# Performance work log

Hardware: AMD Instinct MI355X
Metric: run time of the kernel (lower is better)

Reference implementation:

```python
import jax, jax.numpy as jnp
import numpy as np

N_STATE = 1024
N_HEAD = 16
DIM_PER_HEAD = N_STATE // N_HEAD  # 64
QK_SCALE = DIM_PER_HEAD ** (-0.5)
B, T, T_CACHE = 8, 256, 768


def setup_inputs() -> dict:
    key = jax.random.key(0)
    ks = jax.random.split(key, 12)
    s = 0.02
    return {
        "x": jax.random.normal(ks[0], (B, T, N_STATE), dtype=jnp.float32),
        "qk_mask": jnp.zeros((T, T_CACHE + T), dtype=jnp.float32),
        "cache_k": jax.random.normal(ks[1], (B, T_CACHE, N_STATE), dtype=jnp.float32),
        "cache_v": jax.random.normal(ks[2], (B, T_CACHE, N_STATE), dtype=jnp.float32),
        "Wq": jax.random.normal(ks[3], (N_STATE, N_STATE), dtype=jnp.float32) * s,
        "bq": jax.random.normal(ks[4], (N_STATE,), dtype=jnp.float32) * s,
        "Wk": jax.random.normal(ks[5], (N_STATE, N_STATE), dtype=jnp.float32) * s,
        "Wv": jax.random.normal(ks[6], (N_STATE, N_STATE), dtype=jnp.float32) * s,
        "bv": jax.random.normal(ks[7], (N_STATE,), dtype=jnp.float32) * s,
        "Wo": jax.random.normal(ks[8], (N_STATE, N_STATE), dtype=jnp.float32) * s,
        "bo": jax.random.normal(ks[9], (N_STATE,), dtype=jnp.float32) * s,
    }


def reference(x, qk_mask, cache_k, cache_v, Wq, bq, Wk, Wv, bv, Wo, bo):
    # Linear projections (weights stored as [in, out], i.e. torch weight^T)
    q = (x @ Wq + bq) * QK_SCALE            # [B, T, D]
    new_k = x @ Wk                           # key has no bias
    new_v = x @ Wv + bv
    # KV-cache concat along time
    k = jnp.concatenate([cache_k, new_k], axis=1)  # [B, Tkv, D]
    v = jnp.concatenate([cache_v, new_v], axis=1)
    # Split heads
    Bq, Tq = q.shape[:2]
    Tkv = k.shape[1]
    qh = q.reshape(Bq, Tq, N_HEAD, DIM_PER_HEAD)    # [B, T, H, d]
    kh = k.reshape(Bq, Tkv, N_HEAD, DIM_PER_HEAD)
    vh = v.reshape(Bq, Tkv, N_HEAD, DIM_PER_HEAD)
    # q @ k^T + mask, softmax over keys
    qk = jnp.einsum("bthd,bshd->bhts", qh, kh) + qk_mask  # [B, H, T, Tkv]
    w = jax.nn.softmax(qk, axis=-1).astype(qh.dtype)
    wv = jnp.einsum("bhts,bshd->bthd", w, vh).reshape(Bq, Tq, N_STATE)
    out = wv @ Wo + bo
    return out, new_k, new_v
```

## Files before the change

kernel.cpp:

```cpp
#include <hip/hip_runtime.h>
#include <hip/hip_bf16.h>
#include <stdint.h>

#define Bb 8
#define Tt 256
#define TCC 768
#define TKV 1024
#define NS 1024
#define NH 16
#define DH 64
#define QK_SCALE 0.125f

typedef short bf16x8 __attribute__((ext_vector_type(8)));
typedef float f32x4 __attribute__((ext_vector_type(4)));

__device__ __forceinline__ unsigned short f2bf(float f) {
  union { float f; uint32_t u; } v; v.f = f;
  uint32_t u = v.u;
  u += 0x7fff + ((u >> 16) & 1);
  return (unsigned short)(u >> 16);
}

__global__ void convert_flat(const float* __restrict__ x, const float* __restrict__ ck,
                             unsigned short* __restrict__ xb, unsigned short* __restrict__ kb) {
  const int64_t nx4 = (int64_t)Bb * Tt * NS / 4;
  const int64_t nk4 = (int64_t)Bb * TCC * NS / 4;
  int64_t stride = (int64_t)gridDim.x * blockDim.x;
  for (int64_t t = (int64_t)blockIdx.x * blockDim.x + threadIdx.x; t < nx4 + nk4; t += stride) {
    if (t < nx4) {
      float4 v = ((const float4*)x)[t];
      ushort4 o; o.x = f2bf(v.x); o.y = f2bf(v.y); o.z = f2bf(v.z); o.w = f2bf(v.w);
      ((ushort4*)xb)[t] = o;
    } else {
      int64_t e = t - nx4;
      float4 v = ((const float4*)ck)[e];
      ushort4 o; o.x = f2bf(v.x); o.y = f2bf(v.y); o.z = f2bf(v.z); o.w = f2bf(v.w);
      int64_t el = e * 4;
      int64_t b = el / ((int64_t)TCC * NS);
      int64_t rem = el % ((int64_t)TCC * NS);
      int64_t d = b * (int64_t)TKV * NS + rem;
      ((ushort4*)kb)[d / 4] = o;
    }
  }
}

__global__ void transpose_convert(const float* __restrict__ Wq, const float* __restrict__ Wk,
                                  const float* __restrict__ Wv, const float* __restrict__ Wo,
                                  const float* __restrict__ cv,
                                  unsigned short* __restrict__ wqt, unsigned short* __restrict__ wkt,
                                  unsigned short* __restrict__ wvt, unsigned short* __restrict__ wot,
                                  unsigned short* __restrict__ vbt) {
  __shared__ float tile[64][65];
  int bid = blockIdx.x;
  const float* src; unsigned short* dst;
  if (bid < 1024) {
    int mat = bid >> 8, t = bid & 255;
    int tr = t >> 4, tc = t & 15;
    const float* W = (mat == 0) ? Wq : (mat == 1) ? Wk : (mat == 2) ? Wv : Wo;
    unsigned short* Wt = (mat == 0) ? wqt : (mat == 1) ? wkt : (mat == 2) ? wvt : wot;
    src = W + (int64_t)(tr * 64) * 1024 + tc * 64;
    dst = Wt + (int64_t)(tc * 64) * 1024 + tr * 64;
  } else {
    int e = bid - 1024;
    int b = e / 192; int t = e % 192;
    int st = t >> 4, ct = t & 15;
    src = cv + (int64_t)b * TCC * NS + (int64_t)(st * 64) * 1024 + ct * 64;
    dst = vbt + (int64_t)b * NS * TKV + (int64_t)(ct * 64) * 1024 + st * 64;
  }
  for (int e = threadIdx.x; e < 4096; e += 256) {
    int i = e >> 6, j = e & 63;
    tile[i][j] = src[(int64_t)i * 1024 + j];
  }
  __syncthreads();
  for (int e = threadIdx.x; e < 4096; e += 256) {
    int i = e >> 6, j = e & 63;
    dst[(int64_t)i * 1024 + j] = f2bf(tile[j][i]);
  }
}

template <int MODE>
__global__ void gemm128(const unsigned short* __restrict__ A,
                        const unsigned short* __restrict__ Bt0, const unsigned short* __restrict__ Bt1,
                        const unsigned short* __restrict__ Bt2,
                        const float* __restrict__ bq, const float* __restrict__ bv,
                        const float* __restrict__ bo,
                        unsigned short* __restrict__ qb,
                        float* __restrict__ okf, float* __restrict__ ovf,
                        unsigned short* __restrict__ kb, unsigned short* __restrict__ vbt,
                        float* __restrict__ outf) {
  __shared__ unsigned short As[128 * 40];
  __shared__ unsigned short Bs[128 * 40];
  int tid = threadIdx.x, lane = tid & 63, w = tid >> 6;
  int lr = lane & 15, hi = lane >> 4;
  int wr = w >> 1, wc = w & 1;

  int tm, seg, col0;
  const unsigned short* Bt;
  if (MODE == 0) {
    tm = blockIdx.x & 15; int tn = blockIdx.x >> 4;
    seg = tn >> 3; col0 = (tn & 7) * 128;
    Bt = (seg == 0) ? Bt0 : (seg == 1) ? Bt1 : Bt2;
  } else {
    tm = blockIdx.x & 15; int tn = blockIdx.x >> 4;
    seg = 0; col0 = tn * 128;
    Bt = Bt0;
  }
  int m0 = tm * 128;

  f32x4 acc[4][4];
#pragma unroll
  for (int i = 0; i < 4; i++)
#pragma unroll
    for (int j = 0; j < 4; j++) acc[i][j] = (f32x4){0.f, 0.f, 0.f, 0.f};

  for (int k0 = 0; k0 < 1024; k0 += 32) {
#pragma unroll
    for (int e = tid; e < 512; e += 256) {
      int r = e >> 2, kc = (e & 3) * 8;
      *(bf16x8*)&As[r * 40 + kc] = *(const bf16x8*)&A[(int64_t)(m0 + r) * 1024 + k0 + kc];
      *(bf16x8*)&Bs[r * 40 + kc] = *(const bf16x8*)&Bt[(int64_t)(col0 + r) * 1024 + k0 + kc];
    }
    __syncthreads();
    bf16x8 af[4], bf[4];
#pragma unroll
    for (int mt = 0; mt < 4; mt++) af[mt] = *(const bf16x8*)&As[(wr * 64 + mt * 16 + lr) * 40 + hi * 8];
#pragma unroll
    for (int nt = 0; nt < 4; nt++) bf[nt] = *(const bf16x8*)&Bs[(wc * 64 + nt * 16 + lr) * 40 + hi * 8];
#pragma unroll
    for (int mt = 0; mt < 4; mt++)
#pragma unroll
      for (int nt = 0; nt < 4; nt++)
        acc[mt][nt] = __builtin_amdgcn_mfma_f32_16x16x32_bf16(af[mt], bf[nt], acc[mt][nt], 0, 0, 0);
    __syncthreads();
  }

#pragma unroll
  for (int mt = 0; mt < 4; mt++)
#pragma unroll
    for (int nt = 0; nt < 4; nt++) {
      int row = m0 + wr * 64 + mt * 16 + hi * 4;
      int col = col0 + wc * 64 + nt * 16 + lr;
      if (MODE == 1) {
        float bias = bo[col];
#pragma unroll
        for (int r = 0; r < 4; r++)
          outf[(int64_t)(row + r) * 1024 + col] = acc[mt][nt][r] + bias;
      } else if (seg == 0) {
        float bias = bq[col];
#pragma unroll
        for (int r = 0; r < 4; r++)
          qb[(int64_t)(row + r) * 1024 + col] = f2bf((acc[mt][nt][r] + bias) * QK_SCALE);
      } else if (seg == 1) {
#pragma unroll
        for (int r = 0; r < 4; r++) {
          float v = acc[mt][nt][r];
          okf[(int64_t)(row + r) * 1024 + col] = v;
          int b = (row + r) >> 8, t = (row + r) & 255;
          kb[((int64_t)(b * TKV + TCC + t)) * 1024 + col] = f2bf(v);
        }
      } else {
        float bias = bv[col];
        int b = row >> 8, t0 = row & 255;
        int64_t voff = ((int64_t)(b * NH + (col >> 6)) * DH + (col & 63)) * TKV + TCC + t0;
        ushort4 pk;
        float v0 = acc[mt][nt][0] + bias, v1 = acc[mt][nt][1] + bias,
              v2 = acc[mt][nt][2] + bias, v3 = acc[mt][nt][3] + bias;
        ovf[(int64_t)(row + 0) * 1024 + col] = v0;
        ovf[(int64_t)(row + 1) * 1024 + col] = v1;
        ovf[(int64_t)(row + 2) * 1024 + col] = v2;
        ovf[(int64_t)(row + 3) * 1024 + col] = v3;
        pk.x = f2bf(v0); pk.y = f2bf(v1); pk.z = f2bf(v2); pk.w = f2bf(v3);
        *(ushort4*)&vbt[voff] = pk;
      }
    }
}

__global__ void attn(const unsigned short* __restrict__ qb, const unsigned short* __restrict__ kb,
                     const unsigned short* __restrict__ vbt, const float* __restrict__ mask,
                     unsigned short* __restrict__ wvb) {
  __shared__ unsigned short Ks[64 * 72];
  __shared__ unsigned short Vs[64 * 72];
  __shared__ unsigned short Ps[4][16 * 72];
  int tid = threadIdx.x, lane = tid & 63, w = tid >> 6;
  int lr = lane & 15, hi = lane >> 4;
  int qblk = blockIdx.x & 3, bh = blockIdx.x >> 2, b = bh >> 4, h = bh & 15;
  int q0 = qblk * 64 + w * 16;

  const unsigned short* qp = qb + ((int64_t)(b * Tt + q0 + lr)) * 1024 + h * DH + hi * 8;
  bf16x8 aq0 = *(const bf16x8*)qp;
  bf16x8 aq1 = *(const bf16x8*)(qp + 32);

  f32x4 o[4];
#pragma unroll
  for (int nt = 0; nt < 4; nt++) o[nt] = (f32x4){0.f, 0.f, 0.f, 0.f};
  float m[4] = {-1e30f, -1e30f, -1e30f, -1e30f};
  float l[4] = {0.f, 0.f, 0.f, 0.f};

  const unsigned short* kbase = kb + (int64_t)b * TKV * 1024 + h * DH;
  const unsigned short* vbase = vbt + (int64_t)bh * DH * TKV;
  const float* mbase = mask + (int64_t)(q0 + hi * 4) * TKV;

  for (int c = 0; c < 16; c++) {
    int kv0 = c * 64;
#pragma unroll
    for (int e = tid; e < 512; e += 256) {
      int r = e >> 3, kc = (e & 7) * 8;
      *(bf16x8*)&Ks[r * 72 + kc] = *(const bf16x8*)&kbase[(int64_t)(kv0 + r) * 1024 + kc];
      *(bf16x8*)&Vs[r * 72 + kc] = *(const bf16x8*)&vbase[(int64_t)r * TKV + kv0 + kc];
    }
    __syncthreads();

    f32x4 s[4];
#pragma unroll
    for (int nt = 0; nt < 4; nt++) {
      bf16x8 bk0 = *(const bf16x8*)&Ks[(nt * 16 + lr) * 72 + hi * 8];
      bf16x8 bk1 = *(const bf16x8*)&Ks[(nt * 16 + lr) * 72 + 32 + hi * 8];
      f32x4 z = (f32x4){0.f, 0.f, 0.f, 0.f};
      z = __builtin_amdgcn_mfma_f32_16x16x32_bf16(aq0, bk0, z, 0, 0, 0);
      z = __builtin_amdgcn_mfma_f32_16x16x32_bf16(aq1, bk1, z, 0, 0, 0);
      s[nt] = z;
    }
#pragma unroll
    for (int nt = 0; nt < 4; nt++)
#pragma unroll
      for (int r = 0; r < 4; r++)
        s[nt][r] += mbase[(int64_t)r * TKV + kv0 + nt * 16 + lr];

    float cm[4];
#pragma unroll
    for (int r = 0; r < 4; r++) {
      cm[r] = fmaxf(fmaxf(s[0][r], s[1][r]), fmaxf(s[2][r], s[3][r]));
#pragma unroll
      for (int d = 1; d < 16; d <<= 1) cm[r] = fmaxf(cm[r], __shfl_xor(cm[r], d));
    }
    float al[4], rs[4];
#pragma unroll
    for (int r = 0; r < 4; r++) {
      float nm = fmaxf(m[r], cm[r]);
      al[r] = __expf(m[r] - nm);
      m[r] = nm;
      rs[r] = 0.f;
    }
#pragma unroll
    for (int nt = 0; nt < 4; nt++)
#pragma unroll
      for (int r = 0; r < 4; r++) {
        s[nt][r] = __expf(s[nt][r] - m[r]);
        rs[r] += s[nt][r];
      }
#pragma unroll
    for (int r = 0; r < 4; r++) {
#pragma unroll
      for (int d = 1; d < 16; d <<= 1) rs[r] += __shfl_xor(rs[r], d);
      l[r] = l[r] * al[r] + rs[r];
    }
#pragma unroll
    for (int nt = 0; nt < 4; nt++)
#pragma unroll
      for (int r = 0; r < 4; r++) o[nt][r] *= al[r];

#pragma unroll
    for (int nt = 0; nt < 4; nt++)
#pragma unroll
      for (int r = 0; r < 4; r++)
        Ps[w][(hi * 4 + r) * 72 + nt * 16 + lr] = f2bf(s[nt][r]);
    __syncthreads();

    bf16x8 pa0 = *(const bf16x8*)&Ps[w][lr * 72 + hi * 8];
    bf16x8 pa1 = *(const bf16x8*)&Ps[w][lr * 72 + 32 + hi * 8];
#pragma unroll
    for (int nt = 0; nt < 4; nt++) {
      bf16x8 bv0 = *(const bf16x8*)&Vs[(nt * 16 + lr) * 72 + hi * 8];
      bf16x8 bv1 = *(const bf16x8*)&Vs[(nt * 16 + lr) * 72 + 32 + hi * 8];
      o[nt] = __builtin_amdgcn_mfma_f32_16x16x32_bf16(pa0, bv0, o[nt], 0, 0, 0);
      o[nt] = __builtin_amdgcn_mfma_f32_16x16x32_bf16(pa1, bv1, o[nt], 0, 0, 0);
    }
    __syncthreads();
  }

  float inv[4];
#pragma unroll
  for (int r = 0; r < 4; r++) inv[r] = 1.f / l[r];
#pragma unroll
  for (int nt = 0; nt < 4; nt++)
#pragma unroll
    for (int r = 0; r < 4; r++)
      wvb[(int64_t)(b * Tt + q0 + hi * 4 + r) * 1024 + h * DH + nt * 16 + lr] =
          f2bf(o[nt][r] * inv[r]);
}

extern "C" void kernel_launch(void* const* d_in, const int* in_sizes, int n_in,
                              void* d_out, int out_size, void* d_ws, size_t ws_size,
                              hipStream_t stream) {
  const float* x    = (const float*)d_in[0];
  const float* mask = (const float*)d_in[1];
  const float* ck   = (const float*)d_in[2];
  const float* cv   = (const float*)d_in[3];
  const float* Wq   = (const float*)d_in[4];
  const float* bq   = (const float*)d_in[5];
  const float* Wk   = (const float*)d_in[6];
  const float* Wv   = (const float*)d_in[7];
  const float* bv   = (const float*)d_in[8];
  const float* Wo   = (const float*)d_in[9];
  const float* bo   = (const float*)d_in[10];

  const int64_t NT = (int64_t)Bb * Tt * NS;
  float* outp = (float*)d_out;
  float* okf  = outp + NT;
  float* ovf  = outp + 2 * NT;

  char* ws = (char*)d_ws;
  unsigned short* xb  = (unsigned short*)(ws);
  unsigned short* wqt = (unsigned short*)(ws + (4LL << 20));
  unsigned short* wkt = (unsigned short*)(ws + (6LL << 20));
  unsigned short* wvt = (unsigned short*)(ws + (8LL << 20));
  unsigned short* wot = (unsigned short*)(ws + (10LL << 20));
  unsigned short* qbw = (unsigned short*)(ws + (12LL << 20));
  unsigned short* kbw = (unsigned short*)(ws + (16LL << 20));
  unsigned short* vbt = (unsigned short*)(ws + (32LL << 20));
  unsigned short* wvb = (unsigned short*)(ws + (48LL << 20));

  convert_flat<<<2048, 256, 0, stream>>>(x, ck, xb, kbw);
  transpose_convert<<<2560, 256, 0, stream>>>(Wq, Wk, Wv, Wo, cv, wqt, wkt, wvt, wot, vbt);
  gemm128<0><<<384, 256, 0, stream>>>(xb, wqt, wkt, wvt, bq, bv, bo,
                                      qbw, okf, ovf, kbw, vbt, outp);
  attn<<<512, 256, 0, stream>>>(qbw, kbw, vbt, mask, wvb);
  gemm128<1><<<128, 256, 0, stream>>>(wvb, wot, wot, wot, bq, bv, bo,
                                      qbw, okf, ovf, kbw, vbt, outp);
}
```

Baseline: 242.7 us.

## Double-buffer GEMM and attention tiles via direct global-to-LDS loads with swizzle

Both GEMMs are retiled to smaller blocks: 64x128 for the QKV projection and 64x64 for the output projection. They now stage K-chunks of 64 into double-buffered LDS using global_load_lds with an XOR-swizzled layout, so the next tile loads while MFMAs run on the current one. The attention kernel likewise double-buffers its K/V tiles, prefetches mask values, and drops the barrier around the per-wave P buffer. Block indices are remapped across the 8 XCDs and the weight/V transposes use vectorized float4/ushort4 accesses. This relies on the compiler inserting correct waits for the async LDS loads, and the smaller tiles reduce per-block data reuse in exchange for more blocks.

```diff
diff --git a/kernel.cpp b/kernel.cpp
--- a/kernel.cpp
+++ b/kernel.cpp
@@ -13,6 +13,7 @@
 
 typedef short bf16x8 __attribute__((ext_vector_type(8)));
 typedef float f32x4 __attribute__((ext_vector_type(4)));
+typedef unsigned int u32;
 
 __device__ __forceinline__ unsigned short f2bf(float f) {
   union { float f; uint32_t u; } v; v.f = f;
@@ -21,8 +22,16 @@
   return (unsigned short)(u >> 16);
 }
 
-__global__ void convert_flat(const float* __restrict__ x, const float* __restrict__ ck,
-                             unsigned short* __restrict__ xb, unsigned short* __restrict__ kb) {
+__device__ __forceinline__ void gload16(const unsigned short* g, unsigned short* l) {
+  __builtin_amdgcn_global_load_lds(
+      (__attribute__((address_space(1))) u32*)g,
+      (__attribute__((address_space(3))) u32*)l,
+      16, 0, 0);
+}
+
+__global__ __launch_bounds__(256) void convert_flat(
+    const float* __restrict__ x, const float* __restrict__ ck,
+    unsigned short* __restrict__ xb, unsigned short* __restrict__ kb) {
   const int64_t nx4 = (int64_t)Bb * Tt * NS / 4;
   const int64_t nk4 = (int64_t)Bb * TCC * NS / 4;
   int64_t stride = (int64_t)gridDim.x * blockDim.x;
@@ -44,12 +53,13 @@
   }
 }
 
-__global__ void transpose_convert(const float* __restrict__ Wq, const float* __restrict__ Wk,
-                                  const float* __restrict__ Wv, const float* __restrict__ Wo,
-                                  const float* __restrict__ cv,
-                                  unsigned short* __restrict__ wqt, unsigned short* __restrict__ wkt,
-                                  unsigned short* __restrict__ wvt, unsigned short* __restrict__ wot,
-                                  unsigned short* __restrict__ vbt) {
+__global__ __launch_bounds__(256) void transpose_convert(
+    const float* __restrict__ Wq, const float* __restrict__ Wk,
+    const float* __restrict__ Wv, const float* __restrict__ Wo,
+    const float* __restrict__ cv,
+    unsigned short* __restrict__ wqt, unsigned short* __restrict__ wkt,
+    unsigned short* __restrict__ wvt, unsigned short* __restrict__ wot,
+    unsigned short* __restrict__ vbt) {
   __shared__ float tile[64][65];
   int bid = blockIdx.x;
   const float* src; unsigned short* dst;
@@ -67,79 +77,117 @@
     src = cv + (int64_t)b * TCC * NS + (int64_t)(st * 64) * 1024 + ct * 64;
     dst = vbt + (int64_t)b * NS * TKV + (int64_t)(ct * 64) * 1024 + st * 64;
   }
-  for (int e = threadIdx.x; e < 4096; e += 256) {
-    int i = e >> 6, j = e & 63;
-    tile[i][j] = src[(int64_t)i * 1024 + j];
+  for (int e = threadIdx.x; e < 1024; e += 256) {
+    int i = e >> 4, j4 = (e & 15) * 4;
+    float4 v = *(const float4*)&src[(int64_t)i * 1024 + j4];
+    tile[i][j4] = v.x; tile[i][j4 + 1] = v.y; tile[i][j4 + 2] = v.z; tile[i][j4 + 3] = v.w;
   }
   __syncthreads();
-  for (int e = threadIdx.x; e < 4096; e += 256) {
-    int i = e >> 6, j = e & 63;
-    dst[(int64_t)i * 1024 + j] = f2bf(tile[j][i]);
+  for (int e = threadIdx.x; e < 1024; e += 256) {
+    int i = e >> 4, j4 = (e & 15) * 4;
+    ushort4 o;
+    o.x = f2bf(tile[j4][i]); o.y = f2bf(tile[j4 + 1][i]);
+    o.z = f2bf(tile[j4 + 2][i]); o.w = f2bf(tile[j4 + 3][i]);
+    *(ushort4*)&dst[(int64_t)i * 1024 + j4] = o;
   }
 }
 
 template <int MODE>
-__global__ void gemm128(const unsigned short* __restrict__ A,
-                        const unsigned short* __restrict__ Bt0, const unsigned short* __restrict__ Bt1,
-                        const unsigned short* __restrict__ Bt2,
-                        const float* __restrict__ bq, const float* __restrict__ bv,
-                        const float* __restrict__ bo,
-                        unsigned short* __restrict__ qb,
-                        float* __restrict__ okf, float* __restrict__ ovf,
-                        unsigned short* __restrict__ kb, unsigned short* __restrict__ vbt,
-                        float* __restrict__ outf) {
-  __shared__ unsigned short As[128 * 40];
-  __shared__ unsigned short Bs[128 * 40];
+__global__ __launch_bounds__(256) void gemm_mfma(
+    const unsigned short* __restrict__ A,
+    const unsigned short* __restrict__ Bt0, const unsigned short* __restrict__ Bt1,
+    const unsigned short* __restrict__ Bt2,
+    const float* __restrict__ bq, const float* __restrict__ bv,
+    const float* __restrict__ bo,
+    unsigned short* __restrict__ qb,
+    float* __restrict__ okf, float* __restrict__ ovf,
+    unsigned short* __restrict__ kb, unsigned short* __restrict__ vbt,
+    float* __restrict__ outf) {
+  constexpr int BM = 64;
+  constexpr int BN = (MODE == 0) ? 128 : 64;
+  constexpr int MT = 2;
+  constexpr int NTf = BN / 32;
+  __shared__ __align__(16) unsigned short As[2][BM * 64];
+  __shared__ __align__(16) unsigned short Bs[2][BN * 64];
+
   int tid = threadIdx.x, lane = tid & 63, w = tid >> 6;
   int lr = lane & 15, hi = lane >> 4;
-  int wr = w >> 1, wc = w & 1;
-
-  int tm, seg, col0;
+  int wm = w >> 1, wn = w & 1;
+
+  int bid = blockIdx.x;
+  int cpx = gridDim.x >> 3;
+  int logical = (bid & 7) * cpx + (bid >> 3);
+
+  int tm = logical & 31;
+  int tn = logical >> 5;
+  int seg, col0;
   const unsigned short* Bt;
   if (MODE == 0) {
-    tm = blockIdx.x & 15; int tn = blockIdx.x >> 4;
     seg = tn >> 3; col0 = (tn & 7) * 128;
     Bt = (seg == 0) ? Bt0 : (seg == 1) ? Bt1 : Bt2;
   } else {
-    tm = blockIdx.x & 15; int tn = blockIdx.x >> 4;
-    seg = 0; col0 = tn * 128;
+    seg = 0; col0 = tn * 64;
     Bt = Bt0;
   }
-  int m0 = tm * 128;
-
-  f32x4 acc[4][4];
-#pragma unroll
-  for (int i = 0; i < 4; i++)
-#pragma unroll
-    for (int j = 0; j < 4; j++) acc[i][j] = (f32x4){0.f, 0.f, 0.f, 0.f};
-
-  for (int k0 = 0; k0 < 1024; k0 += 32) {
-#pragma unroll
-    for (int e = tid; e < 512; e += 256) {
-      int r = e >> 2, kc = (e & 3) * 8;
-      *(bf16x8*)&As[r * 40 + kc] = *(const bf16x8*)&A[(int64_t)(m0 + r) * 1024 + k0 + kc];
-      *(bf16x8*)&Bs[r * 40 + kc] = *(const bf16x8*)&Bt[(int64_t)(col0 + r) * 1024 + k0 + kc];
-    }
+  int m0 = tm * 64;
+
+  int srow = lane >> 3;
+  int sch8 = (((lane & 7) ^ srow)) * 8;
+  int sw = lr & 7;
+
+  f32x4 acc[MT][NTf];
+#pragma unroll
+  for (int i = 0; i < MT; i++)
+#pragma unroll
+    for (int j = 0; j < NTf; j++) acc[i][j] = (f32x4){0.f, 0.f, 0.f, 0.f};
+
+  auto STAGE = [&](int buf, int k0) {
+#pragma unroll
+    for (int i = 0; i < 2; i++) {
+      int rb = w * 16 + i * 8;
+      gload16(&A[(int64_t)(m0 + rb + srow) * 1024 + k0 + sch8], &As[buf][rb * 64]);
+    }
+#pragma unroll
+    for (int i = 0; i < BN / 32; i++) {
+      int rb = w * (BN / 4) + i * 8;
+      gload16(&Bt[(int64_t)(col0 + rb + srow) * 1024 + k0 + sch8], &Bs[buf][rb * 64]);
+    }
+  };
+
+  STAGE(0, 0);
+  __syncthreads();
+  int cur = 0;
+  for (int step = 0; step < 16; ++step) {
+    if (step < 15) STAGE(cur ^ 1, (step + 1) * 64);
+    bf16x8 af[2][MT], bfr[2][NTf];
+#pragma unroll
+    for (int kk = 0; kk < 2; kk++) {
+      int ch = ((kk * 4 + hi) ^ sw) * 8;
+#pragma unroll
+      for (int mt = 0; mt < MT; mt++)
+        af[kk][mt] = *(const bf16x8*)&As[cur][(wm * 32 + mt * 16 + lr) * 64 + ch];
+#pragma unroll
+      for (int nt = 0; nt < NTf; nt++)
+        bfr[kk][nt] = *(const bf16x8*)&Bs[cur][(wn * (BN / 2) + nt * 16 + lr) * 64 + ch];
+    }
+#pragma unroll
+    for (int kk = 0; kk < 2; kk++)
+#pragma unroll
+      for (int mt = 0; mt < MT; mt++)
+#pragma unroll
+        for (int nt = 0; nt < NTf; nt++)
+          acc[mt][nt] = __builtin_amdgcn_mfma_f32_16x16x32_bf16(af[kk][mt], bfr[kk][nt],
+                                                               acc[mt][nt], 0, 0, 0);
     __syncthreads();
-    bf16x8 af[4], bf[4];
-#pragma unroll
-    for (int mt = 0; mt < 4; mt++) af[mt] = *(const bf16x8*)&As[(wr * 64 + mt * 16 + lr) * 40 + hi * 8];
-#pragma unroll
-    for (int nt = 0; nt < 4; nt++) bf[nt] = *(const bf16x8*)&Bs[(wc * 64 + nt * 16 + lr) * 40 + hi * 8];
-#pragma unroll
-    for (int mt = 0; mt < 4; mt++)
-#pragma unroll
-      for (int nt = 0; nt < 4; nt++)
-        acc[mt][nt] = __builtin_amdgcn_mfma_f32_16x16x32_bf16(af[mt], bf[nt], acc[mt][nt], 0, 0, 0);
-    __syncthreads();
-  }
-
-#pragma unroll
-  for (int mt = 0; mt < 4; mt++)
-#pragma unroll
-    for (int nt = 0; nt < 4; nt++) {
-      int row = m0 + wr * 64 + mt * 16 + hi * 4;
-      int col = col0 + wc * 64 + nt * 16 + lr;
+    cur ^= 1;
+  }
+
+#pragma unroll
+  for (int mt = 0; mt < MT; mt++)
+#pragma unroll
+    for (int nt = 0; nt < NTf; nt++) {
+      int row = m0 + wm * 32 + mt * 16 + hi * 4;
+      int col = col0 + wn * (BN / 2) + nt * 16 + lr;
       if (MODE == 1) {
         float bias = bo[col];
 #pragma unroll
@@ -162,29 +210,32 @@
         float bias = bv[col];
         int b = row >> 8, t0 = row & 255;
         int64_t voff = ((int64_t)(b * NH + (col >> 6)) * DH + (col & 63)) * TKV + TCC + t0;
-        ushort4 pk;
         float v0 = acc[mt][nt][0] + bias, v1 = acc[mt][nt][1] + bias,
               v2 = acc[mt][nt][2] + bias, v3 = acc[mt][nt][3] + bias;
         ovf[(int64_t)(row + 0) * 1024 + col] = v0;
         ovf[(int64_t)(row + 1) * 1024 + col] = v1;
         ovf[(int64_t)(row + 2) * 1024 + col] = v2;
         ovf[(int64_t)(row + 3) * 1024 + col] = v3;
-        pk.x = f2bf(v0); pk.y = f2bf(v1); pk.z = f2bf(v2); pk.w = f2bf(v3);
+        ushort4 pk; pk.x = f2bf(v0); pk.y = f2bf(v1); pk.z = f2bf(v2); pk.w = f2bf(v3);
         *(ushort4*)&vbt[voff] = pk;
       }
     }
 }
 
-__global__ void attn(const unsigned short* __restrict__ qb, const unsigned short* __restrict__ kb,
-                     const unsigned short* __restrict__ vbt, const float* __restrict__ mask,
-                     unsigned short* __restrict__ wvb) {
-  __shared__ unsigned short Ks[64 * 72];
-  __shared__ unsigned short Vs[64 * 72];
-  __shared__ unsigned short Ps[4][16 * 72];
+__global__ __launch_bounds__(256) void attn(
+    const unsigned short* __restrict__ qb, const unsigned short* __restrict__ kb,
+    const unsigned short* __restrict__ vbt, const float* __restrict__ mask,
+    unsigned short* __restrict__ wvb) {
+  __shared__ __align__(16) unsigned short Ks[2][64 * 64];
+  __shared__ __align__(16) unsigned short Vs[2][64 * 64];
+  __shared__ unsigned short Ps[4][16 * 76];
+
   int tid = threadIdx.x, lane = tid & 63, w = tid >> 6;
   int lr = lane & 15, hi = lane >> 4;
-  int qblk = blockIdx.x & 3, bh = blockIdx.x >> 2, b = bh >> 4, h = bh & 15;
-  int q0 = qblk * 64 + w * 16;
+  int bid = blockIdx.x;
+  int logical = (bid & 7) * 64 + (bid >> 3);
+  int qt = logical & 3, bh = logical >> 2, b = bh >> 4, h = bh & 15;
+  int q0 = qt * 64 + w * 16;
 
   const unsigned short* qp = qb + ((int64_t)(b * Tt + q0 + lr)) * 1024 + h * DH + hi * 8;
   bf16x8 aq0 = *(const bf16x8*)qp;
@@ -200,21 +251,40 @@
   const unsigned short* vbase = vbt + (int64_t)bh * DH * TKV;
   const float* mbase = mask + (int64_t)(q0 + hi * 4) * TKV;
 
-  for (int c = 0; c < 16; c++) {
+  int srow = lane >> 3;
+  int sch8 = ((lane & 7) ^ srow) * 8;
+  int sw = lr & 7;
+
+  auto STAGE = [&](int buf, int kv0) {
+#pragma unroll
+    for (int i = 0; i < 2; i++) {
+      int rb = w * 16 + i * 8;
+      gload16(&kbase[(int64_t)(kv0 + rb + srow) * 1024 + sch8], &Ks[buf][rb * 64]);
+      gload16(&vbase[(int64_t)(rb + srow) * TKV + kv0 + sch8], &Vs[buf][rb * 64]);
+    }
+  };
+
+  STAGE(0, 0);
+  __syncthreads();
+  int cur = 0;
+  for (int c = 0; c < 16; ++c) {
     int kv0 = c * 64;
-#pragma unroll
-    for (int e = tid; e < 512; e += 256) {
-      int r = e >> 3, kc = (e & 7) * 8;
-      *(bf16x8*)&Ks[r * 72 + kc] = *(const bf16x8*)&kbase[(int64_t)(kv0 + r) * 1024 + kc];
-      *(bf16x8*)&Vs[r * 72 + kc] = *(const bf16x8*)&vbase[(int64_t)r * TKV + kv0 + kc];
-    }
-    __syncthreads();
-
+    if (c < 15) STAGE(cur ^ 1, kv0 + 64);
+
+    float mk[4][4];
+#pragma unroll
+    for (int nt = 0; nt < 4; nt++)
+#pragma unroll
+      for (int r = 0; r < 4; r++)
+        mk[nt][r] = mbase[(int64_t)r * TKV + kv0 + nt * 16 + lr];
+
+    int ch0 = (hi ^ sw) * 8, ch1 = ((hi + 4) ^ sw) * 8;
     f32x4 s[4];
 #pragma unroll
     for (int nt = 0; nt < 4; nt++) {
-      bf16x8 bk0 = *(const bf16x8*)&Ks[(nt * 16 + lr) * 72 + hi * 8];
-      bf16x8 bk1 = *(const bf16x8*)&Ks[(nt * 16 + lr) * 72 + 32 + hi * 8];
+      int row = (nt * 16 + lr) * 64;
+      bf16x8 bk0 = *(const bf16x8*)&Ks[cur][row + ch0];
+      bf16x8 bk1 = *(const bf16x8*)&Ks[cur][row + ch1];
       f32x4 z = (f32x4){0.f, 0.f, 0.f, 0.f};
       z = __builtin_amdgcn_mfma_f32_16x16x32_bf16(aq0, bk0, z, 0, 0, 0);
       z = __builtin_amdgcn_mfma_f32_16x16x32_bf16(aq1, bk1, z, 0, 0, 0);
@@ -223,8 +293,7 @@
 #pragma unroll
     for (int nt = 0; nt < 4; nt++)
 #pragma unroll
-      for (int r = 0; r < 4; r++)
-        s[nt][r] += mbase[(int64_t)r * TKV + kv0 + nt * 16 + lr];
+      for (int r = 0; r < 4; r++) s[nt][r] += mk[nt][r];
 
     float cm[4];
 #pragma unroll
@@ -263,19 +332,20 @@
     for (int nt = 0; nt < 4; nt++)
 #pragma unroll
       for (int r = 0; r < 4; r++)
-        Ps[w][(hi * 4 + r) * 72 + nt * 16 + lr] = f2bf(s[nt][r]);
-    __syncthreads();
-
-    bf16x8 pa0 = *(const bf16x8*)&Ps[w][lr * 72 + hi * 8];
-    bf16x8 pa1 = *(const bf16x8*)&Ps[w][lr * 72 + 32 + hi * 8];
+        Ps[w][(hi * 4 + r) * 76 + nt * 16 + lr] = f2bf(s[nt][r]);
+    bf16x8 pa0 = *(const bf16x8*)&Ps[w][lr * 76 + hi * 8];
+    bf16x8 pa1 = *(const bf16x8*)&Ps[w][lr * 76 + 32 + hi * 8];
+
 #pragma unroll
     for (int nt = 0; nt < 4; nt++) {
-      bf16x8 bv0 = *(const bf16x8*)&Vs[(nt * 16 + lr) * 72 + hi * 8];
-      bf16x8 bv1 = *(const bf16x8*)&Vs[(nt * 16 + lr) * 72 + 32 + hi * 8];
+      int row = (nt * 16 + lr) * 64;
+      bf16x8 bv0 = *(const bf16x8*)&Vs[cur][row + ch0];
+      bf16x8 bv1 = *(const bf16x8*)&Vs[cur][row + ch1];
       o[nt] = __builtin_amdgcn_mfma_f32_16x16x32_bf16(pa0, bv0, o[nt], 0, 0, 0);
       o[nt] = __builtin_amdgcn_mfma_f32_16x16x32_bf16(pa1, bv1, o[nt], 0, 0, 0);
     }
     __syncthreads();
+    cur ^= 1;
   }
 
   float inv[4];
@@ -322,9 +392,9 @@
 
   convert_flat<<<2048, 256, 0, stream>>>(x, ck, xb, kbw);
   transpose_convert<<<2560, 256, 0, stream>>>(Wq, Wk, Wv, Wo, cv, wqt, wkt, wvt, wot, vbt);
-  gemm128<0><<<384, 256, 0, stream>>>(xb, wqt, wkt, wvt, bq, bv, bo,
-                                      qbw, okf, ovf, kbw, vbt, outp);
+  gemm_mfma<0><<<768, 256, 0, stream>>>(xb, wqt, wkt, wvt, bq, bv, bo,
+                                        qbw, okf, ovf, kbw, vbt, outp);
   attn<<<512, 256, 0, stream>>>(qbw, kbw, vbt, mask, wvb);
-  gemm128<1><<<128, 256, 0, stream>>>(wvb, wot, wot, wot, bq, bv, bo,
-                                      qbw, okf, ovf, kbw, vbt, outp);
-}
+  gemm_mfma<1><<<512, 256, 0, stream>>>(wvb, wot, wot, wot, bq, bv, bo,
+                                        qbw, okf, ovf, kbw, vbt, outp);
+}
```

New measurement: 211.5 us. 1.15x faster.
